# Performance work log

Hardware: AMD Instinct MI355X
Metric: run time of the kernel (lower is better)

The kernel has to match this reference:

```python
import jax, jax.numpy as jnp
import numpy as np

B, L, C, H = 8, 1024, 512, 8
D = C // H  # head_size = 64


def setup_inputs() -> dict:
    key = jax.random.key(0)
    k1, k2, k3, k4, k5, k6 = jax.random.split(key, 6)
    x = jax.random.normal(k1, (B, L, C), dtype=jnp.float32)
    adj = jax.random.randint(k2, (B, L, L), 0, 2).astype(jnp.float32)
    distance = jax.random.randint(k3, (B, L, L), 0, 3).astype(jnp.float32)
    # nn.Linear(dim, 3*dim, bias=False): stored as y = x @ W; init ~ U(-1/sqrt(C), 1/sqrt(C))
    bound = 1.0 / np.sqrt(C)
    w_qkv = jax.random.uniform(k4, (C, 3 * C), minval=-bound, maxval=bound, dtype=jnp.float32)
    w_proj = jax.random.uniform(k5, (C, C), minval=-bound, maxval=bound, dtype=jnp.float32)
    # struct_gamma is zero-init in the module; use small random values so biases are exercised
    gamma = 0.1 * jax.random.normal(k6, (H, 5), dtype=jnp.float32)
    return {"x": x, "adj": adj, "distance": distance,
            "w_qkv": w_qkv, "w_proj": w_proj, "gamma": gamma}


def reference(x, adj, distance, w_qkv, w_proj, gamma):
    b, l, c = x.shape
    scale = jnp.asarray(np.sqrt(D), x.dtype)
    qkv = x @ w_qkv                                    # [B,L,3C]
    q, k, v = jnp.split(qkv, 3, axis=-1)
    q = q.reshape(b, l, H, D).transpose(0, 2, 1, 3)     # [B,H,L,D]
    k = k.reshape(b, l, H, D).transpose(0, 2, 1, 3)
    v = v.reshape(b, l, H, D).transpose(0, 2, 1, 3)
    s = jnp.einsum('bhid,bhjd->bhij', q, k) / scale     # [B,H,L,L]

    # has_cls=True: zero row 0 and col 0 of adj
    adj_local = adj.at[:, 0, :].set(0.0).at[:, :, 0].set(0.0)
    adj_t = adj_local.transpose(0, 2, 1)
    b_fwd = adj_local                                   # direct edges
    b_bwd = adj_t
    b_dist_fwd = (distance > 0).astype(x.dtype)         # multi-hop reachability
    b_dist_bwd = (distance.transpose(0, 2, 1) > 0).astype(x.dtype)
    b_struct = (jnp.einsum('bik,bjk->bij', adj_local, adj_local) > 0).astype(x.dtype)

    biases = jnp.stack([b_fwd, b_bwd, b_dist_fwd, b_dist_bwd, b_struct], axis=1)  # [B,5,L,L]
    s = s + jnp.einsum('hk,bkij->bhij', gamma, biases)

    attn = jax.nn.softmax(s, axis=-1)
    out = jnp.einsum('bhij,bhjd->bhid', attn, v)        # [B,H,L,D]
    out = out.transpose(0, 2, 1, 3).reshape(b, l, c)
    return out @ w_proj
```

## Files before the change

kernel.cpp:

```cpp
#include <hip/hip_runtime.h>
#include <hip/hip_bf16.h>
#include <stdint.h>

#define NB 8
#define NL 1024
#define NC 512
#define NH 8
#define ND 64

typedef __attribute__((ext_vector_type(8))) short short8;
typedef __attribute__((ext_vector_type(4))) float f32x4;
typedef unsigned long long u64;

__device__ __forceinline__ short f2bf(float f) {
  union { float f; uint32_t u; } v; v.f = f;
  uint32_t r = v.u + 0x7FFFu + ((v.u >> 16) & 1u);
  return (short)(r >> 16);
}

#if __has_builtin(__builtin_amdgcn_exp2f)
#define EXP2(x) __builtin_amdgcn_exp2f(x)
#else
#define EXP2(x) exp2f(x)
#endif

#define MFMA16(a, b, c) __builtin_amdgcn_mfma_f32_16x16x32_bf16((a), (b), (c), 0, 0, 0)

__global__ __launch_bounds__(256) void pack_k(const float* __restrict__ adj,
                                              const float* __restrict__ dist,
                                              u64* __restrict__ padj,
                                              u64* __restrict__ pdist) {
  int row = blockIdx.x;
  int i = row & (NL - 1);
  int wv = threadIdx.x >> 6, lane = threadIdx.x & 63;
  const float* asrc = adj + (size_t)row * NL;
  const float* dsrc = dist + (size_t)row * NL;
  #pragma unroll
  for (int it = 0; it < 4; it++) {
    int j = wv * 256 + it * 64 + lane;
    float a = asrc[j];
    float d = dsrc[j];
    u64 am = __ballot((a != 0.0f) && (i != 0) && (j != 0));
    u64 dm = __ballot(d > 0.0f);
    if (lane == 0) {
      padj[(size_t)row * 16 + wv * 4 + it] = am;
      pdist[(size_t)row * 16 + wv * 4 + it] = dm;
    }
  }
}

__global__ __launch_bounds__(256) void bits_k(const u64* __restrict__ padj,
                                              const u64* __restrict__ pdist,
                                              unsigned char* __restrict__ bits) {
  __shared__ u64 Pi[64][17], Pj[64][17];
  __shared__ u64 DiW[64], DjW[64];
  int b = blockIdx.z, i0 = blockIdx.y * 64, j0 = blockIdx.x * 64;
  int t = threadIdx.x;
  int jw = j0 >> 6, iw = i0 >> 6;
  const u64* pa = padj + (size_t)b * NL * 16;
  const u64* pd = pdist + (size_t)b * NL * 16;
  #pragma unroll
  for (int s = 0; s < 4; s++) {
    int idx = s * 256 + t; int r = idx >> 4, w = idx & 15;
    Pi[r][w] = pa[(size_t)(i0 + r) * 16 + w];
    Pj[r][w] = pa[(size_t)(j0 + r) * 16 + w];
  }
  if (t < 64) DiW[t] = pd[(size_t)(i0 + t) * 16 + jw];
  else if (t < 128) DjW[t - 64] = pd[(size_t)(j0 + t - 64) * 16 + iw];
  __syncthreads();
  const size_t base = (size_t)b * NL * NL;
  int jj0 = (t & 15) * 4;
  #pragma unroll
  for (int s = 0; s < 4; s++) {
    int ii = (t >> 4) + s * 16;
    u64 fwdw = Pi[ii][jw];
    u64 dfw = DiW[ii];
    uint32_t acc = 0;
    #pragma unroll
    for (int q = 0; q < 4; q++) {
      int jj = jj0 + q;
      unsigned v = 0;
      v |= (unsigned)((fwdw >> jj) & 1);
      v |= (unsigned)((Pj[jj][iw] >> ii) & 1) << 1;
      v |= (unsigned)((dfw >> jj) & 1) << 2;
      v |= (unsigned)((DjW[jj] >> ii) & 1) << 3;
      #pragma unroll 1
      for (int w = 0; w < 16; w++) {
        if (Pi[ii][w] & Pj[jj][w]) { v |= 16; break; }
      }
      acc |= v << (8 * q);
    }
    *(uint32_t*)&bits[base + (size_t)(i0 + ii) * NL + j0 + jj0] = acc;
  }
}

__global__ __launch_bounds__(256) void wcvt_k(const float* __restrict__ w,
                                              unsigned short* __restrict__ wt,
                                              int Ndim) {
  __shared__ short T[64][68];
  int k0 = blockIdx.y * 64, n0 = blockIdx.x * 64;
  int t = threadIdx.x;
  {
    int r = t >> 2, c0 = (t & 3) * 16;
    const float* src = w + (size_t)(k0 + r) * Ndim + n0 + c0;
    float4 a0 = *(const float4*)src;
    float4 a1 = *(const float4*)(src + 4);
    float4 a2 = *(const float4*)(src + 8);
    float4 a3 = *(const float4*)(src + 12);
    short8 s0, s1;
    s0[0] = f2bf(a0.x); s0[1] = f2bf(a0.y); s0[2] = f2bf(a0.z); s0[3] = f2bf(a0.w);
    s0[4] = f2bf(a1.x); s0[5] = f2bf(a1.y); s0[6] = f2bf(a1.z); s0[7] = f2bf(a1.w);
    s1[0] = f2bf(a2.x); s1[1] = f2bf(a2.y); s1[2] = f2bf(a2.z); s1[3] = f2bf(a2.w);
    s1[4] = f2bf(a3.x); s1[5] = f2bf(a3.y); s1[6] = f2bf(a3.z); s1[7] = f2bf(a3.w);
    *(short8*)&T[r][c0]     = s0;
    *(short8*)&T[r][c0 + 8] = s1;
  }
  __syncthreads();
  #pragma unroll
  for (int it = 0; it < 2; it++) {
    int nn = (t >> 3) + it * 32, kc = (t & 7) * 8;
    short8 v;
    #pragma unroll
    for (int j = 0; j < 8; j++) v[j] = T[kc + j][nn];
    *(short8*)(wt + (size_t)(n0 + nn) * NC + k0 + kc) = v;
  }
}

__global__ __launch_bounds__(256) void qkv_gemm_k(const float* __restrict__ x,
                                                  const unsigned short* __restrict__ wqT,
                                                  unsigned short* __restrict__ qb,
                                                  unsigned short* __restrict__ kb,
                                                  unsigned short* __restrict__ vb) {
  __shared__ short Al[64][40];
  __shared__ short Bl[64][40];
  int t = threadIdx.x;
  int wv = t >> 6, lane = t & 63, lg = lane >> 4, lm = lane & 15;
  int wr = wv >> 1, wc = wv & 1;
  int M0 = blockIdx.y * 64, N0 = blockIdx.x * 64;
  f32x4 zero4 = {0.f, 0.f, 0.f, 0.f};
  f32x4 acc[2][2] = {{zero4, zero4}, {zero4, zero4}};
  for (int k0 = 0; k0 < NC; k0 += 32) {
    {
      int row = t >> 2, cc = (t & 3) * 8;
      const float* src = x + (size_t)(M0 + row) * NC + k0 + cc;
      float4 v0 = *(const float4*)src;
      float4 v1 = *(const float4*)(src + 4);
      short8 s8;
      s8[0] = f2bf(v0.x); s8[1] = f2bf(v0.y); s8[2] = f2bf(v0.z); s8[3] = f2bf(v0.w);
      s8[4] = f2bf(v1.x); s8[5] = f2bf(v1.y); s8[6] = f2bf(v1.z); s8[7] = f2bf(v1.w);
      *(short8*)&Al[row][cc] = s8;
    }
    {
      int n = t >> 2, kk = (t & 3) * 8;
      *(short8*)&Bl[n][kk] =
          *(const short8*)(wqT + (size_t)(N0 + n) * NC + k0 + kk);
    }
    __syncthreads();
    short8 af[2], bfr[2];
    af[0] = *(short8*)&Al[wr * 32 + lm][lg * 8];
    af[1] = *(short8*)&Al[wr * 32 + 16 + lm][lg * 8];
    bfr[0] = *(short8*)&Bl[wc * 32 + lm][lg * 8];
    bfr[1] = *(short8*)&Bl[wc * 32 + 16 + lm][lg * 8];
    #pragma unroll
    for (int mi = 0; mi < 2; mi++)
      #pragma unroll
      for (int ni = 0; ni < 2; ni++)
        acc[mi][ni] = MFMA16(af[mi], bfr[ni], acc[mi][ni]);
    __syncthreads();
  }
  #pragma unroll
  for (int mi = 0; mi < 2; mi++)
    #pragma unroll
    for (int ni = 0; ni < 2; ni++)
      #pragma unroll
      for (int r = 0; r < 4; r++) {
        int m = M0 + wr * 32 + mi * 16 + lg * 4 + r;
        int n = N0 + wc * 32 + ni * 16 + lm;
        int which = n >> 9, c = n & 511;
        int h = c >> 6, d = c & 63;
        int bb = m >> 10, ll = m & 1023;
        float val = acc[mi][ni][r];
        unsigned short* dst;
        if (which == 0) { dst = qb; val *= 0.125f; }
        else dst = (which == 1) ? kb : vb;
        dst[(((size_t)bb * NH + h) * NL + ll) * ND + d] = (unsigned short)f2bf(val);
      }
}

__global__ __launch_bounds__(256) void vt_k(const unsigned short* __restrict__ vb,
                                            unsigned short* __restrict__ vtb) {
  __shared__ short T[64][68];
  int b = blockIdx.z, h = blockIdx.y, l0 = blockIdx.x * 64;
  int t = threadIdx.x;
  const size_t bh = (size_t)b * NH + h;
  {
    int r = t >> 2, c0 = (t & 3) * 16;
    const unsigned short* src = vb + ((bh * NL) + l0 + r) * ND + c0;
    *(short8*)&T[r][c0]     = *(const short8*)src;
    *(short8*)&T[r][c0 + 8] = *(const short8*)(src + 8);
  }
  __syncthreads();
  #pragma unroll
  for (int it = 0; it < 2; it++) {
    int d = (t >> 3) + it * 32, lc = (t & 7) * 8;
    short8 v;
    #pragma unroll
    for (int j = 0; j < 8; j++) v[j] = T[lc + j][d];
    *(short8*)(vtb + (bh * ND + d) * NL + l0 + lc) = v;
  }
}

__global__ __launch_bounds__(256) void attn_k(const unsigned short* __restrict__ qb,
                                              const unsigned short* __restrict__ kb,
                                              const unsigned short* __restrict__ vtb,
                                              const unsigned char* __restrict__ bits,
                                              const float* __restrict__ gamma,
                                              unsigned short* __restrict__ ao) {
  __shared__ short Kl[64][72];
  __shared__ short Vt[64][72];
  __shared__ short Pl[64][68];
  __shared__ float lut[32];
  int b = blockIdx.z, h = blockIdx.y, q0 = blockIdx.x * 64;
  int t = threadIdx.x, wv = t >> 6, lane = t & 63, lg = lane >> 4, lm = lane & 15;
  const float LOG2E = 1.4426950408889634f;
  if (t < 32) {
    float s = 0.f;
    #pragma unroll
    for (int k = 0; k < 5; k++) if ((t >> k) & 1) s += gamma[h * 5 + k];
    lut[t] = s * LOG2E - 8.0f;
  }
  const size_t bh = ((size_t)b * NH + h) * NL;
  const size_t bhD = ((size_t)b * NH + h) * ND;
  short8 qf[2];
  {
    const unsigned short* src = qb + (bh + q0 + wv * 16 + lm) * ND + lg * 8;
    qf[0] = *(const short8*)src;
    qf[1] = *(const short8*)(src + 32);
  }
  f32x4 zero4 = {0.f, 0.f, 0.f, 0.f};
  f32x4 oacc[4] = {zero4, zero4, zero4, zero4};
  float lsum[4] = {0.f, 0.f, 0.f, 0.f};
  __syncthreads();
  for (int j0 = 0; j0 < NL; j0 += 64) {
    {
      int r = t >> 2, cc = (t & 3) * 16;
      const unsigned short* ks = kb + (bh + j0 + r) * ND + cc;
      *(short8*)&Kl[r][cc]     = *(const short8*)ks;
      *(short8*)&Kl[r][cc + 8] = *(const short8*)(ks + 8);
      const unsigned short* vs = vtb + (bhD + r) * NL + j0 + cc;
      *(short8*)&Vt[r][cc]     = *(const short8*)vs;
      *(short8*)&Vt[r][cc + 8] = *(const short8*)(vs + 8);
    }
    __syncthreads();
    f32x4 sf[4];
    #pragma unroll
    for (int ni = 0; ni < 4; ni++) {
      short8 b0 = *(short8*)&Kl[ni * 16 + lm][lg * 8];
      short8 b1 = *(short8*)&Kl[ni * 16 + lm][32 + lg * 8];
      f32x4 c = {0.f, 0.f, 0.f, 0.f};
      c = MFMA16(qf[0], b0, c);
      c = MFMA16(qf[1], b1, c);
      sf[ni] = c;
    }
    #pragma unroll
    for (int ni = 0; ni < 4; ni++)
      #pragma unroll
      for (int r = 0; r < 4; r++) {
        int qi = q0 + wv * 16 + lg * 4 + r;
        int kj = j0 + ni * 16 + lm;
        unsigned char bt = bits[((size_t)b * NL + qi) * NL + kj];
        float p = EXP2(fmaf(sf[ni][r], LOG2E, lut[bt & 31]));
        lsum[r] += p;
        Pl[wv * 16 + lg * 4 + r][ni * 16 + lm] = f2bf(p);
      }
    short8 pa0 = *(short8*)&Pl[wv * 16 + lm][lg * 8];
    short8 pa1 = *(short8*)&Pl[wv * 16 + lm][32 + lg * 8];
    #pragma unroll
    for (int di = 0; di < 4; di++) {
      short8 vb0 = *(short8*)&Vt[di * 16 + lm][lg * 8];
      short8 vb1 = *(short8*)&Vt[di * 16 + lm][32 + lg * 8];
      oacc[di] = MFMA16(pa0, vb0, oacc[di]);
      oacc[di] = MFMA16(pa1, vb1, oacc[di]);
    }
    __syncthreads();
  }
  float inv[4];
  #pragma unroll
  for (int r = 0; r < 4; r++) {
    float s = lsum[r];
    s += __shfl_xor(s, 1);
    s += __shfl_xor(s, 2);
    s += __shfl_xor(s, 4);
    s += __shfl_xor(s, 8);
    inv[r] = 1.0f / s;
  }
  #pragma unroll
  for (int di = 0; di < 4; di++)
    #pragma unroll
    for (int r = 0; r < 4; r++) {
      int qi = q0 + wv * 16 + lg * 4 + r;
      int d = di * 16 + lm;
      ao[((size_t)b * NL + qi) * NC + h * ND + d] =
          (unsigned short)f2bf(oacc[di][r] * inv[r]);
    }
}

__global__ __launch_bounds__(256) void proj_gemm_k(const unsigned short* __restrict__ ao,
                                                   const unsigned short* __restrict__ wpT,
                                                   float* __restrict__ out) {
  __shared__ short Al[64][40];
  __shared__ short Bl[64][40];
  int t = threadIdx.x;
  int wv = t >> 6, lane = t & 63, lg = lane >> 4, lm = lane & 15;
  int wr = wv >> 1, wc = wv & 1;
  int M0 = blockIdx.y * 64, N0 = blockIdx.x * 64;
  f32x4 zero4 = {0.f, 0.f, 0.f, 0.f};
  f32x4 acc[2][2] = {{zero4, zero4}, {zero4, zero4}};
  for (int k0 = 0; k0 < NC; k0 += 32) {
    {
      int row = t >> 2, cc = (t & 3) * 8;
      *(short8*)&Al[row][cc] = *(const short8*)(ao + (size_t)(M0 + row) * NC + k0 + cc);
    }
    {
      int n = t >> 2, kk = (t & 3) * 8;
      *(short8*)&Bl[n][kk] =
          *(const short8*)(wpT + (size_t)(N0 + n) * NC + k0 + kk);
    }
    __syncthreads();
    short8 af[2], bfr[2];
    af[0] = *(short8*)&Al[wr * 32 + lm][lg * 8];
    af[1] = *(short8*)&Al[wr * 32 + 16 + lm][lg * 8];
    bfr[0] = *(short8*)&Bl[wc * 32 + lm][lg * 8];
    bfr[1] = *(short8*)&Bl[wc * 32 + 16 + lm][lg * 8];
    #pragma unroll
    for (int mi = 0; mi < 2; mi++)
      #pragma unroll
      for (int ni = 0; ni < 2; ni++)
        acc[mi][ni] = MFMA16(af[mi], bfr[ni], acc[mi][ni]);
    __syncthreads();
  }
  #pragma unroll
  for (int mi = 0; mi < 2; mi++)
    #pragma unroll
    for (int ni = 0; ni < 2; ni++)
      #pragma unroll
      for (int r = 0; r < 4; r++) {
        int m = M0 + wr * 32 + mi * 16 + lg * 4 + r;
        int n = N0 + wc * 32 + ni * 16 + lm;
        out[(size_t)m * NC + n] = acc[mi][ni][r];
      }
}

extern "C" void kernel_launch(void* const* d_in, const int* in_sizes, int n_in,
                              void* d_out, int out_size, void* d_ws, size_t ws_size,
                              hipStream_t stream) {
  (void)in_sizes; (void)n_in; (void)out_size; (void)ws_size;
  const float* x      = (const float*)d_in[0];
  const float* adj    = (const float*)d_in[1];
  const float* dist   = (const float*)d_in[2];
  const float* w_qkv  = (const float*)d_in[3];
  const float* w_proj = (const float*)d_in[4];
  const float* gamma  = (const float*)d_in[5];
  float* out = (float*)d_out;

  char* ws = (char*)d_ws;
  size_t off = 0;
  auto take = [&](size_t bytes) -> char* {
    char* p = ws + off;
    off += (bytes + 255) & ~(size_t)255;
    return p;
  };
  unsigned short* qb = (unsigned short*)take((size_t)NB * NH * NL * ND * 2);
  unsigned short* kb = (unsigned short*)take((size_t)NB * NH * NL * ND * 2);
  unsigned short* vb = (unsigned short*)take((size_t)NB * NH * NL * ND * 2);
  unsigned short* vtb = (unsigned short*)take((size_t)NB * NH * NL * ND * 2);
  u64* padj  = (u64*)take((size_t)NB * NL * 16 * 8);
  u64* pdist = (u64*)take((size_t)NB * NL * 16 * 8);
  unsigned char* bits = (unsigned char*)take((size_t)NB * NL * NL);
  unsigned short* ao = (unsigned short*)take((size_t)NB * NL * NC * 2);
  unsigned short* wqT = (unsigned short*)take((size_t)3 * NC * NC * 2);
  unsigned short* wpT = (unsigned short*)take((size_t)NC * NC * 2);

  pack_k<<<dim3(NB * NL), dim3(256), 0, stream>>>(adj, dist, padj, pdist);
  wcvt_k<<<dim3(24, 8), dim3(256), 0, stream>>>(w_qkv, wqT, 3 * NC);
  wcvt_k<<<dim3(8, 8), dim3(256), 0, stream>>>(w_proj, wpT, NC);
  qkv_gemm_k<<<dim3(24, 128), dim3(256), 0, stream>>>(x, wqT, qb, kb, vb);
  vt_k<<<dim3(16, NH, NB), dim3(256), 0, stream>>>(vb, vtb);
  bits_k<<<dim3(16, 16, NB), dim3(256), 0, stream>>>(padj, pdist, bits);
  attn_k<<<dim3(16, NH, NB), dim3(256), 0, stream>>>(qb, kb, vtb, bits, gamma, ao);
  proj_gemm_k<<<dim3(8, 128), dim3(256), 0, stream>>>(ao, wpT, out);
}
```

Baseline: 268.0 us.

## Pre-convert x to bf16, enlarge QKV GEMM tiles, restructure attention with transposed MFMA

A new kernel converts x to bf16 once, so the QKV GEMM no longer converts it on every tile load. The QKV GEMM tile grows from 64x64 to 128x128, giving 16 MFMAs per wave per k-step for more operand reuse. The attention kernel now runs 2 waves of 32 query rows each and computes S^T and O^T by swapping MFMA operands. This allows 4-byte vectorized loads of the bits mask, packed P stores to LDS, and 4-wide output stores. The xb buffer is reused as the attention output, and the larger GEMM tiles leave fewer blocks and add register pressure.

```diff
diff --git a/kernel.cpp b/kernel.cpp
--- a/kernel.cpp
+++ b/kernel.cpp
@@ -9,6 +9,7 @@
 #define ND 64
 
 typedef __attribute__((ext_vector_type(8))) short short8;
+typedef __attribute__((ext_vector_type(4))) short short4v;
 typedef __attribute__((ext_vector_type(4))) float f32x4;
 typedef unsigned long long u64;
 
@@ -126,56 +127,63 @@
   }
 }
 
-__global__ __launch_bounds__(256) void qkv_gemm_k(const float* __restrict__ x,
+__global__ __launch_bounds__(256) void xcvt_k(const float* __restrict__ x,
+                                              unsigned short* __restrict__ xb) {
+  size_t i = ((size_t)blockIdx.x * 256 + threadIdx.x) * 8;
+  float4 a0 = *(const float4*)(x + i);
+  float4 a1 = *(const float4*)(x + i + 4);
+  short8 s;
+  s[0] = f2bf(a0.x); s[1] = f2bf(a0.y); s[2] = f2bf(a0.z); s[3] = f2bf(a0.w);
+  s[4] = f2bf(a1.x); s[5] = f2bf(a1.y); s[6] = f2bf(a1.z); s[7] = f2bf(a1.w);
+  *(short8*)(xb + i) = s;
+}
+
+__global__ __launch_bounds__(256) void qkv_gemm_k(const unsigned short* __restrict__ xb,
                                                   const unsigned short* __restrict__ wqT,
                                                   unsigned short* __restrict__ qb,
                                                   unsigned short* __restrict__ kb,
                                                   unsigned short* __restrict__ vb) {
-  __shared__ short Al[64][40];
-  __shared__ short Bl[64][40];
+  __shared__ short Al[128][40];
+  __shared__ short Bl[128][40];
   int t = threadIdx.x;
   int wv = t >> 6, lane = t & 63, lg = lane >> 4, lm = lane & 15;
   int wr = wv >> 1, wc = wv & 1;
-  int M0 = blockIdx.y * 64, N0 = blockIdx.x * 64;
+  int M0 = blockIdx.y * 128, N0 = blockIdx.x * 128;
   f32x4 zero4 = {0.f, 0.f, 0.f, 0.f};
-  f32x4 acc[2][2] = {{zero4, zero4}, {zero4, zero4}};
+  f32x4 acc[4][4];
+  #pragma unroll
+  for (int mi = 0; mi < 4; mi++)
+    #pragma unroll
+    for (int ni = 0; ni < 4; ni++) acc[mi][ni] = zero4;
+  int srow = t & 127, scc = (t >> 7) * 16;
   for (int k0 = 0; k0 < NC; k0 += 32) {
-    {
-      int row = t >> 2, cc = (t & 3) * 8;
-      const float* src = x + (size_t)(M0 + row) * NC + k0 + cc;
-      float4 v0 = *(const float4*)src;
-      float4 v1 = *(const float4*)(src + 4);
-      short8 s8;
-      s8[0] = f2bf(v0.x); s8[1] = f2bf(v0.y); s8[2] = f2bf(v0.z); s8[3] = f2bf(v0.w);
-      s8[4] = f2bf(v1.x); s8[5] = f2bf(v1.y); s8[6] = f2bf(v1.z); s8[7] = f2bf(v1.w);
-      *(short8*)&Al[row][cc] = s8;
-    }
-    {
-      int n = t >> 2, kk = (t & 3) * 8;
-      *(short8*)&Bl[n][kk] =
-          *(const short8*)(wqT + (size_t)(N0 + n) * NC + k0 + kk);
-    }
-    __syncthreads();
-    short8 af[2], bfr[2];
-    af[0] = *(short8*)&Al[wr * 32 + lm][lg * 8];
-    af[1] = *(short8*)&Al[wr * 32 + 16 + lm][lg * 8];
-    bfr[0] = *(short8*)&Bl[wc * 32 + lm][lg * 8];
-    bfr[1] = *(short8*)&Bl[wc * 32 + 16 + lm][lg * 8];
-    #pragma unroll
-    for (int mi = 0; mi < 2; mi++)
-      #pragma unroll
-      for (int ni = 0; ni < 2; ni++)
+    const unsigned short* as = xb + (size_t)(M0 + srow) * NC + k0 + scc;
+    *(short8*)&Al[srow][scc]     = *(const short8*)as;
+    *(short8*)&Al[srow][scc + 8] = *(const short8*)(as + 8);
+    const unsigned short* bs = wqT + (size_t)(N0 + srow) * NC + k0 + scc;
+    *(short8*)&Bl[srow][scc]     = *(const short8*)bs;
+    *(short8*)&Bl[srow][scc + 8] = *(const short8*)(bs + 8);
+    __syncthreads();
+    short8 af[4], bfr[4];
+    #pragma unroll
+    for (int mi = 0; mi < 4; mi++) af[mi] = *(short8*)&Al[wr * 64 + mi * 16 + lm][lg * 8];
+    #pragma unroll
+    for (int ni = 0; ni < 4; ni++) bfr[ni] = *(short8*)&Bl[wc * 64 + ni * 16 + lm][lg * 8];
+    #pragma unroll
+    for (int mi = 0; mi < 4; mi++)
+      #pragma unroll
+      for (int ni = 0; ni < 4; ni++)
         acc[mi][ni] = MFMA16(af[mi], bfr[ni], acc[mi][ni]);
     __syncthreads();
   }
   #pragma unroll
-  for (int mi = 0; mi < 2; mi++)
-    #pragma unroll
-    for (int ni = 0; ni < 2; ni++)
+  for (int mi = 0; mi < 4; mi++)
+    #pragma unroll
+    for (int ni = 0; ni < 4; ni++)
       #pragma unroll
       for (int r = 0; r < 4; r++) {
-        int m = M0 + wr * 32 + mi * 16 + lg * 4 + r;
-        int n = N0 + wc * 32 + ni * 16 + lm;
+        int m = M0 + wr * 64 + mi * 16 + lg * 4 + r;
+        int n = N0 + wc * 64 + ni * 16 + lm;
         int which = n >> 9, c = n & 511;
         int h = c >> 6, d = c & 63;
         int bb = m >> 10, ll = m & 1023;
@@ -210,7 +218,7 @@
   }
 }
 
-__global__ __launch_bounds__(256) void attn_k(const unsigned short* __restrict__ qb,
+__global__ __launch_bounds__(128) void attn_k(const unsigned short* __restrict__ qb,
                                               const unsigned short* __restrict__ kb,
                                               const unsigned short* __restrict__ vtb,
                                               const unsigned char* __restrict__ bits,
@@ -218,7 +226,7 @@
                                               unsigned short* __restrict__ ao) {
   __shared__ short Kl[64][72];
   __shared__ short Vt[64][72];
-  __shared__ short Pl[64][68];
+  __shared__ short Pl[64][72];
   __shared__ float lut[32];
   int b = blockIdx.z, h = blockIdx.y, q0 = blockIdx.x * 64;
   int t = threadIdx.x, wv = t >> 6, lane = t & 63, lg = lane >> 4, lm = lane & 15;
@@ -231,77 +239,106 @@
   }
   const size_t bh = ((size_t)b * NH + h) * NL;
   const size_t bhD = ((size_t)b * NH + h) * ND;
-  short8 qf[2];
-  {
-    const unsigned short* src = qb + (bh + q0 + wv * 16 + lm) * ND + lg * 8;
-    qf[0] = *(const short8*)src;
-    qf[1] = *(const short8*)(src + 32);
+  short8 qf[2][2];
+  #pragma unroll
+  for (int mi = 0; mi < 2; mi++) {
+    const unsigned short* src = qb + (bh + q0 + wv * 32 + mi * 16 + lm) * ND + lg * 8;
+    qf[mi][0] = *(const short8*)src;
+    qf[mi][1] = *(const short8*)(src + 32);
   }
   f32x4 zero4 = {0.f, 0.f, 0.f, 0.f};
-  f32x4 oacc[4] = {zero4, zero4, zero4, zero4};
-  float lsum[4] = {0.f, 0.f, 0.f, 0.f};
+  f32x4 oaccT[4][2];
+  #pragma unroll
+  for (int di = 0; di < 4; di++) { oaccT[di][0] = zero4; oaccT[di][1] = zero4; }
+  float lsum[2] = {0.f, 0.f};
+  int sr = t >> 1, sc = (t & 1) * 32;
+  const unsigned short* krow = kb + (bh + sr) * ND + sc;
+  const unsigned short* vrow = vtb + (bhD + sr) * NL + sc;
   __syncthreads();
-  for (int j0 = 0; j0 < NL; j0 += 64) {
+  for (int ti = 0; ti < 16; ti++) {
+    int j0 = ti * 64;
     {
-      int r = t >> 2, cc = (t & 3) * 16;
-      const unsigned short* ks = kb + (bh + j0 + r) * ND + cc;
-      *(short8*)&Kl[r][cc]     = *(const short8*)ks;
-      *(short8*)&Kl[r][cc + 8] = *(const short8*)(ks + 8);
-      const unsigned short* vs = vtb + (bhD + r) * NL + j0 + cc;
-      *(short8*)&Vt[r][cc]     = *(const short8*)vs;
-      *(short8*)&Vt[r][cc + 8] = *(const short8*)(vs + 8);
-    }
-    __syncthreads();
-    f32x4 sf[4];
+      const unsigned short* ks = krow + (size_t)j0 * ND;
+      *(short8*)&Kl[sr][sc]      = *(const short8*)ks;
+      *(short8*)&Kl[sr][sc + 8]  = *(const short8*)(ks + 8);
+      *(short8*)&Kl[sr][sc + 16] = *(const short8*)(ks + 16);
+      *(short8*)&Kl[sr][sc + 24] = *(const short8*)(ks + 24);
+      const unsigned short* vs = vrow + j0;
+      *(short8*)&Vt[sr][sc]      = *(const short8*)vs;
+      *(short8*)&Vt[sr][sc + 8]  = *(const short8*)(vs + 8);
+      *(short8*)&Vt[sr][sc + 16] = *(const short8*)(vs + 16);
+      *(short8*)&Vt[sr][sc + 24] = *(const short8*)(vs + 24);
+    }
+    __syncthreads();
+    f32x4 sfT[2][4];
     #pragma unroll
     for (int ni = 0; ni < 4; ni++) {
-      short8 b0 = *(short8*)&Kl[ni * 16 + lm][lg * 8];
-      short8 b1 = *(short8*)&Kl[ni * 16 + lm][32 + lg * 8];
-      f32x4 c = {0.f, 0.f, 0.f, 0.f};
-      c = MFMA16(qf[0], b0, c);
-      c = MFMA16(qf[1], b1, c);
-      sf[ni] = c;
-    }
-    #pragma unroll
-    for (int ni = 0; ni < 4; ni++)
-      #pragma unroll
-      for (int r = 0; r < 4; r++) {
-        int qi = q0 + wv * 16 + lg * 4 + r;
-        int kj = j0 + ni * 16 + lm;
-        unsigned char bt = bits[((size_t)b * NL + qi) * NL + kj];
-        float p = EXP2(fmaf(sf[ni][r], LOG2E, lut[bt & 31]));
-        lsum[r] += p;
-        Pl[wv * 16 + lg * 4 + r][ni * 16 + lm] = f2bf(p);
-      }
-    short8 pa0 = *(short8*)&Pl[wv * 16 + lm][lg * 8];
-    short8 pa1 = *(short8*)&Pl[wv * 16 + lm][32 + lg * 8];
+      short8 kf0 = *(short8*)&Kl[ni * 16 + lm][lg * 8];
+      short8 kf1 = *(short8*)&Kl[ni * 16 + lm][32 + lg * 8];
+      #pragma unroll
+      for (int mi = 0; mi < 2; mi++) {
+        f32x4 c = {0.f, 0.f, 0.f, 0.f};
+        c = MFMA16(kf0, qf[mi][0], c);
+        c = MFMA16(kf1, qf[mi][1], c);
+        sfT[mi][ni] = c;
+      }
+    }
+    #pragma unroll
+    for (int mi = 0; mi < 2; mi++) {
+      int qrow = q0 + wv * 32 + mi * 16 + lm;
+      const unsigned char* bp = bits + ((size_t)b * NL + qrow) * NL + j0 + 4 * lg;
+      int prow = wv * 32 + mi * 16 + lm;
+      #pragma unroll
+      for (int ni = 0; ni < 4; ni++) {
+        uint32_t bw = *(const uint32_t*)(bp + ni * 16);
+        float p0 = EXP2(fmaf(sfT[mi][ni][0], LOG2E, lut[bw & 31]));
+        float p1 = EXP2(fmaf(sfT[mi][ni][1], LOG2E, lut[(bw >> 8) & 31]));
+        float p2 = EXP2(fmaf(sfT[mi][ni][2], LOG2E, lut[(bw >> 16) & 31]));
+        float p3 = EXP2(fmaf(sfT[mi][ni][3], LOG2E, lut[(bw >> 24) & 31]));
+        lsum[mi] += (p0 + p1) + (p2 + p3);
+        uint32_t d0 = (uint32_t)(unsigned short)f2bf(p0) |
+                      ((uint32_t)(unsigned short)f2bf(p1) << 16);
+        uint32_t d1 = (uint32_t)(unsigned short)f2bf(p2) |
+                      ((uint32_t)(unsigned short)f2bf(p3) << 16);
+        *(uint32_t*)&Pl[prow][ni * 16 + 4 * lg]     = d0;
+        *(uint32_t*)&Pl[prow][ni * 16 + 4 * lg + 2] = d1;
+      }
+    }
+    short8 pf[2][2];
+    #pragma unroll
+    for (int mi = 0; mi < 2; mi++) {
+      pf[mi][0] = *(short8*)&Pl[wv * 32 + mi * 16 + lm][lg * 8];
+      pf[mi][1] = *(short8*)&Pl[wv * 32 + mi * 16 + lm][32 + lg * 8];
+    }
     #pragma unroll
     for (int di = 0; di < 4; di++) {
-      short8 vb0 = *(short8*)&Vt[di * 16 + lm][lg * 8];
-      short8 vb1 = *(short8*)&Vt[di * 16 + lm][32 + lg * 8];
-      oacc[di] = MFMA16(pa0, vb0, oacc[di]);
-      oacc[di] = MFMA16(pa1, vb1, oacc[di]);
-    }
-    __syncthreads();
-  }
-  float inv[4];
-  #pragma unroll
-  for (int r = 0; r < 4; r++) {
-    float s = lsum[r];
-    s += __shfl_xor(s, 1);
-    s += __shfl_xor(s, 2);
-    s += __shfl_xor(s, 4);
-    s += __shfl_xor(s, 8);
-    inv[r] = 1.0f / s;
+      short8 vf0 = *(short8*)&Vt[di * 16 + lm][lg * 8];
+      short8 vf1 = *(short8*)&Vt[di * 16 + lm][32 + lg * 8];
+      #pragma unroll
+      for (int mi = 0; mi < 2; mi++) {
+        oaccT[di][mi] = MFMA16(vf0, pf[mi][0], oaccT[di][mi]);
+        oaccT[di][mi] = MFMA16(vf1, pf[mi][1], oaccT[di][mi]);
+      }
+    }
+    __syncthreads();
+  }
+  float inv[2];
+  #pragma unroll
+  for (int mi = 0; mi < 2; mi++) {
+    float s = lsum[mi];
+    s += __shfl_xor(s, 16);
+    s += __shfl_xor(s, 32);
+    inv[mi] = 1.0f / s;
   }
   #pragma unroll
   for (int di = 0; di < 4; di++)
     #pragma unroll
-    for (int r = 0; r < 4; r++) {
-      int qi = q0 + wv * 16 + lg * 4 + r;
-      int d = di * 16 + lm;
-      ao[((size_t)b * NL + qi) * NC + h * ND + d] =
-          (unsigned short)f2bf(oacc[di][r] * inv[r]);
+    for (int mi = 0; mi < 2; mi++) {
+      int qi = q0 + wv * 32 + mi * 16 + lm;
+      short4v o;
+      #pragma unroll
+      for (int r = 0; r < 4; r++) o[r] = f2bf(oaccT[di][mi][r] * inv[mi]);
+      *(short4v*)(ao + ((size_t)b * NL + qi) * NC + h * ND + di * 16 + 4 * lg) = o;
     }
 }
 
@@ -377,16 +414,18 @@
   u64* padj  = (u64*)take((size_t)NB * NL * 16 * 8);
   u64* pdist = (u64*)take((size_t)NB * NL * 16 * 8);
   unsigned char* bits = (unsigned char*)take((size_t)NB * NL * NL);
-  unsigned short* ao = (unsigned short*)take((size_t)NB * NL * NC * 2);
+  unsigned short* xb = (unsigned short*)take((size_t)NB * NL * NC * 2);
+  unsigned short* ao = xb;
   unsigned short* wqT = (unsigned short*)take((size_t)3 * NC * NC * 2);
   unsigned short* wpT = (unsigned short*)take((size_t)NC * NC * 2);
 
   pack_k<<<dim3(NB * NL), dim3(256), 0, stream>>>(adj, dist, padj, pdist);
   wcvt_k<<<dim3(24, 8), dim3(256), 0, stream>>>(w_qkv, wqT, 3 * NC);
   wcvt_k<<<dim3(8, 8), dim3(256), 0, stream>>>(w_proj, wpT, NC);
-  qkv_gemm_k<<<dim3(24, 128), dim3(256), 0, stream>>>(x, wqT, qb, kb, vb);
+  xcvt_k<<<dim3((NB * NL * NC) / (256 * 8)), dim3(256), 0, stream>>>(x, xb);
+  qkv_gemm_k<<<dim3(12, 64), dim3(256), 0, stream>>>(xb, wqT, qb, kb, vb);
   vt_k<<<dim3(16, NH, NB), dim3(256), 0, stream>>>(vb, vtb);
   bits_k<<<dim3(16, 16, NB), dim3(256), 0, stream>>>(padj, pdist, bits);
-  attn_k<<<dim3(16, NH, NB), dim3(256), 0, stream>>>(qb, kb, vtb, bits, gamma, ao);
+  attn_k<<<dim3(16, NH, NB), dim3(128), 0, stream>>>(qb, kb, vtb, bits, gamma, ao);
   proj_gemm_k<<<dim3(8, 128), dim3(256), 0, stream>>>(ao, wpT, out);
 }
```

After: 287.8 us. 7.4% more time.
